# Kernel tuning notes

Hardware: AMD Instinct MI355X
Metric: run time of the kernel (lower is better)

Reference implementation:

```python
import jax, jax.numpy as jnp
import numpy as np

B, T, D, H = 8, 1024, 1024, 16
HD = D // H  # head_dim = 64


def setup_inputs() -> dict:
    key = jax.random.key(0)
    ks = jax.random.split(key, 3)
    scale = 0.02
    return {
        "x": jax.random.normal(ks[0], (B, T, D), dtype=jnp.float32),
        "w_qkv": jax.random.normal(ks[1], (D, 3 * D), dtype=jnp.float32) * scale,
        "b_qkv": jnp.zeros((3 * D,), dtype=jnp.float32),
        "w_proj": jax.random.normal(ks[2], (D, D), dtype=jnp.float32) * scale,
        "b_proj": jnp.zeros((D,), dtype=jnp.float32),
    }


def reference(x, w_qkv, b_qkv, w_proj, b_proj):
    b, t, c = x.shape
    qkv = x @ w_qkv + b_qkv                      # [B,T,3D]
    qkv = qkv.reshape(b, t, 3, H, HD)
    q, k, v = [jnp.transpose(qkv[:, :, i], (0, 2, 1, 3)) for i in range(3)]  # [B,H,T,HD]
    att = jnp.einsum("bhqd,bhkd->bhqk", q, k) / np.sqrt(HD)
    causal = jnp.triu(jnp.ones((t, t), dtype=bool), k=1)
    att = jnp.where(causal, -jnp.inf, att)
    att = jax.nn.softmax(att, axis=-1)
    out = jnp.einsum("bhqk,bhkd->bhqd", att, v)  # [B,H,T,HD]
    out = jnp.transpose(out, (0, 2, 1, 3)).reshape(b, t, c)
    return out @ w_proj + b_proj
```

## Files before the change

### kernel.cpp

```cpp
#include <hip/hip_runtime.h>
#include <hip/hip_bf16.h>

#define BATCH 8
#define SEQ   1024
#define DIM   1024
#define NH    16
#define HDIM  64
#define LDQKV 3072

typedef __attribute__((ext_vector_type(8))) short bf16x8;
typedef __attribute__((ext_vector_type(4))) float f32x4;

typedef const __attribute__((address_space(1))) void* gvptr;
typedef __attribute__((address_space(3))) void* lvptr;

static __device__ __forceinline__ short f2bf(float f) {
    unsigned u = __float_as_uint(f);
    unsigned r = (u + 0x7fffu + ((u >> 16) & 1u)) >> 16;
    return (short)r;
}
static __device__ __forceinline__ unsigned pack2bf(float lo, float hi) {
    unsigned a = __float_as_uint(lo), b = __float_as_uint(hi);
    return ((a + 0x8000u) >> 16) | ((b + 0x8000u) & 0xffff0000u);
}

__global__ __launch_bounds__(256) void cast_f2b_kernel(
    const float* __restrict__ in, short* __restrict__ out)
{
    size_t i = ((size_t)blockIdx.x * 256 + threadIdx.x) * 8;
    float4 a = *(const float4*)&in[i];
    float4 b = *(const float4*)&in[i + 4];
    bf16x8 o;
    o[0] = f2bf(a.x); o[1] = f2bf(a.y); o[2] = f2bf(a.z); o[3] = f2bf(a.w);
    o[4] = f2bf(b.x); o[5] = f2bf(b.y); o[6] = f2bf(b.z); o[7] = f2bf(b.w);
    *(bf16x8*)&out[i] = o;
}

__global__ __launch_bounds__(256) void tcast_kernel(
    const float* __restrict__ in, short* __restrict__ out, int R, int C)
{
    __shared__ float Ld[32][33];
    const int tx = threadIdx.x & 31;
    const int ty = threadIdx.x >> 5;
    const int c0 = blockIdx.x * 32;
    const int r0 = blockIdx.y * 32;
#pragma unroll
    for (int i = 0; i < 4; i++) {
        int r = ty + i * 8;
        Ld[r][tx] = in[(size_t)(r0 + r) * C + c0 + tx];
    }
    __syncthreads();
#pragma unroll
    for (int i = 0; i < 4; i++) {
        int rr = ty + i * 8;
        out[(size_t)(c0 + rr) * R + r0 + tx] = f2bf(Ld[tx][rr]);
    }
}

template<bool OUT_BF16>
__global__ __launch_bounds__(256) void gemm_mfma_kernel(
    const short* __restrict__ A,
    const short* __restrict__ Bt,
    const float* __restrict__ bias,
    void* __restrict__ Cout,
    int M, int N, int K)
{
    __shared__ __align__(16) short As[128 * 32];
    __shared__ __align__(16) short Bs[128 * 32];

    const int tid  = threadIdx.x;
    const int w    = tid >> 6;
    const int lane = tid & 63;
    const int l16  = lane & 15;
    const int quad = lane >> 4;
    const int wm   = w >> 1;
    const int wn   = w & 1;
    const int m0   = blockIdx.y * 128;
    const int n0   = blockIdx.x * 128;

    f32x4 acc[4][4];
#pragma unroll
    for (int mi = 0; mi < 4; mi++)
#pragma unroll
        for (int ni = 0; ni < 4; ni++) acc[mi][ni] = (f32x4){0.f, 0.f, 0.f, 0.f};

    for (int kt = 0; kt < K; kt += 32) {
        __syncthreads();
#pragma unroll
        for (int r = 0; r < 2; r++) {
            int vi  = tid + r * 256;
            int row = vi >> 2;
            int kb  = (vi & 3) * 8;
            __builtin_amdgcn_global_load_lds(
                (gvptr)&A[(size_t)(m0 + row) * K + kt + kb],
                (lvptr)&As[vi * 8], 16, 0, 0);
        }
#pragma unroll
        for (int r = 0; r < 2; r++) {
            int vi  = tid + r * 256;
            int row = vi >> 2;
            int kb  = (vi & 3) * 8;
            __builtin_amdgcn_global_load_lds(
                (gvptr)&Bt[(size_t)(n0 + row) * K + kt + kb],
                (lvptr)&Bs[vi * 8], 16, 0, 0);
        }
        __syncthreads();

        bf16x8 af[4], bfr[4];
#pragma unroll
        for (int mi = 0; mi < 4; mi++)
            af[mi] = *(const bf16x8*)&As[(wm * 64 + mi * 16 + l16) * 32 + quad * 8];
#pragma unroll
        for (int ni = 0; ni < 4; ni++)
            bfr[ni] = *(const bf16x8*)&Bs[(wn * 64 + ni * 16 + l16) * 32 + quad * 8];
#pragma unroll
        for (int mi = 0; mi < 4; mi++)
#pragma unroll
            for (int ni = 0; ni < 4; ni++)
                acc[mi][ni] = __builtin_amdgcn_mfma_f32_16x16x32_bf16(
                    af[mi], bfr[ni], acc[mi][ni], 0, 0, 0);
    }

#pragma unroll
    for (int ni = 0; ni < 4; ni++) {
        int n = n0 + wn * 64 + ni * 16 + l16;
        float bv = bias[n];
#pragma unroll
        for (int mi = 0; mi < 4; mi++) {
#pragma unroll
            for (int reg = 0; reg < 4; reg++) {
                int m = m0 + wm * 64 + mi * 16 + quad * 4 + reg;
                float v = acc[mi][ni][reg] + bv;
                if (OUT_BF16)
                    ((short*)Cout)[(size_t)m * N + n] = f2bf(v);
                else
                    ((float*)Cout)[(size_t)m * N + n] = v;
            }
        }
    }
}

#define LDK 72
#define LDP 72

__global__ __launch_bounds__(256, 4) void attn_kernel(
    const short* __restrict__ qkv, short* __restrict__ out)
{
    const int bh    = blockIdx.x;
    const int qtile = 7 - (int)blockIdx.y;
    const int b  = bh >> 4;
    const int h  = bh & 15;
    const int q0 = qtile * 128;
    const int tid  = threadIdx.x;
    const int w    = tid >> 6;
    const int lane = tid & 63;
    const int l16  = lane & 15;
    const int quad = lane >> 4;

    __shared__ __align__(16) short Ks[64 * LDK];
    __shared__ __align__(16) short Vt[64 * LDK];
    __shared__ __align__(16) short QP[128 * LDP];

    const short* qbase = qkv + (size_t)(b * SEQ + q0) * LDQKV + h * HDIM;
#pragma unroll
    for (int s = 0; s < 4; s++) {
        int vi = tid + s * 256;
        int row = vi >> 3, d8 = (vi & 7) * 8;
        *(bf16x8*)&QP[row * LDP + d8] =
            *(const bf16x8*)&qbase[(size_t)row * LDQKV + d8];
    }
    __syncthreads();

    bf16x8 qfragT[2][2];
#pragma unroll
    for (int qb = 0; qb < 2; qb++)
#pragma unroll
        for (int ks = 0; ks < 2; ks++)
            qfragT[qb][ks] = *(const bf16x8*)
                &QP[(w * 32 + qb * 16 + l16) * LDP + ks * 32 + quad * 8];

    f32x4 o_accT[2][4];
#pragma unroll
    for (int qb = 0; qb < 2; qb++)
#pragma unroll
        for (int db = 0; db < 4; db++) o_accT[qb][db] = (f32x4){0.f, 0.f, 0.f, 0.f};
    float l_run[2] = {0.f, 0.f};

    const int nkt = 2 * qtile + 2;
    const short* kb0 = qkv + (size_t)b * SEQ * LDQKV + DIM + h * HDIM;
    const short* vb0 = kb0 + DIM;

    const int vkey0 = (tid & 15) * 4;
    const int vd4   = (tid >> 4) * 4;

    bf16x8 kreg[2];
    short4 vreg[4];
#pragma unroll
    for (int s = 0; s < 2; s++) {
        int vi = tid + s * 256;
        kreg[s] = *(const bf16x8*)&kb0[(size_t)(vi >> 3) * LDQKV + (vi & 7) * 8];
    }
#pragma unroll
    for (int i = 0; i < 4; i++)
        vreg[i] = *(const short4*)&vb0[(size_t)(vkey0 + i) * LDQKV + vd4];
#pragma unroll
    for (int s = 0; s < 2; s++) {
        int vi = tid + s * 256;
        *(bf16x8*)&Ks[(vi >> 3) * LDK + (vi & 7) * 8] = kreg[s];
    }
    *(short4*)&Vt[(vd4 + 0) * LDK + vkey0] = make_short4(vreg[0].x, vreg[1].x, vreg[2].x, vreg[3].x);
    *(short4*)&Vt[(vd4 + 1) * LDK + vkey0] = make_short4(vreg[0].y, vreg[1].y, vreg[2].y, vreg[3].y);
    *(short4*)&Vt[(vd4 + 2) * LDK + vkey0] = make_short4(vreg[0].z, vreg[1].z, vreg[2].z, vreg[3].z);
    *(short4*)&Vt[(vd4 + 3) * LDK + vkey0] = make_short4(vreg[0].w, vreg[1].w, vreg[2].w, vreg[3].w);

    for (int kt = 0; kt < nkt; kt++) {
        __syncthreads();
        const int k0 = kt * 64;

        if (kt + 1 < nkt) {
            const short* kb = kb0 + (size_t)(k0 + 64) * LDQKV;
            const short* vb = vb0 + (size_t)(k0 + 64) * LDQKV;
#pragma unroll
            for (int s = 0; s < 2; s++) {
                int vi = tid + s * 256;
                kreg[s] = *(const bf16x8*)&kb[(size_t)(vi >> 3) * LDQKV + (vi & 7) * 8];
            }
#pragma unroll
            for (int i = 0; i < 4; i++)
                vreg[i] = *(const short4*)&vb[(size_t)(vkey0 + i) * LDQKV + vd4];
        }

        f32x4 sT[2][4];
#pragma unroll
        for (int qb = 0; qb < 2; qb++)
#pragma unroll
            for (int kb = 0; kb < 4; kb++) sT[qb][kb] = (f32x4){0.f, 0.f, 0.f, 0.f};
#pragma unroll
        for (int kb = 0; kb < 4; kb++) {
            bf16x8 kf0 = *(const bf16x8*)&Ks[(kb * 16 + l16) * LDK + quad * 8];
            bf16x8 kf1 = *(const bf16x8*)&Ks[(kb * 16 + l16) * LDK + 32 + quad * 8];
#pragma unroll
            for (int qb = 0; qb < 2; qb++) {
                sT[qb][kb] = __builtin_amdgcn_mfma_f32_16x16x32_bf16(
                    kf0, qfragT[qb][0], sT[qb][kb], 0, 0, 0);
                sT[qb][kb] = __builtin_amdgcn_mfma_f32_16x16x32_bf16(
                    kf1, qfragT[qb][1], sT[qb][kb], 0, 0, 0);
            }
        }

        const bool domask = (kt >= nkt - 2);
#pragma unroll
        for (int qb = 0; qb < 2; qb++) {
            const int q = q0 + w * 32 + qb * 16 + l16;
            float lsum = 0.f;
#pragma unroll
            for (int kb = 0; kb < 4; kb++) {
                float p[4];
#pragma unroll
                for (int r = 0; r < 4; r++) {
                    float e = __expf(sT[qb][kb][r] * 0.125f);
                    int key = k0 + kb * 16 + quad * 4 + r;
                    p[r] = (!domask || key <= q) ? e : 0.f;
                    lsum += p[r];
                }
                unsigned d0 = pack2bf(p[0], p[1]);
                unsigned d1 = pack2bf(p[2], p[3]);
                *(uint2*)&QP[(w * 32 + qb * 16 + l16) * LDP + kb * 16 + quad * 4] =
                    make_uint2(d0, d1);
            }
            lsum += __shfl_xor(lsum, 16, 64);
            lsum += __shfl_xor(lsum, 32, 64);
            l_run[qb] += lsum;
        }

#pragma unroll
        for (int ks2 = 0; ks2 < 2; ks2++) {
            bf16x8 pf[2];
#pragma unroll
            for (int qb = 0; qb < 2; qb++)
                pf[qb] = *(const bf16x8*)
                    &QP[(w * 32 + qb * 16 + l16) * LDP + ks2 * 32 + quad * 8];
#pragma unroll
            for (int db = 0; db < 4; db++) {
                bf16x8 vf = *(const bf16x8*)&Vt[(db * 16 + l16) * LDK + ks2 * 32 + quad * 8];
#pragma unroll
                for (int qb = 0; qb < 2; qb++)
                    o_accT[qb][db] = __builtin_amdgcn_mfma_f32_16x16x32_bf16(
                        vf, pf[qb], o_accT[qb][db], 0, 0, 0);
            }
        }

        __syncthreads();
        if (kt + 1 < nkt) {
#pragma unroll
            for (int s = 0; s < 2; s++) {
                int vi = tid + s * 256;
                *(bf16x8*)&Ks[(vi >> 3) * LDK + (vi & 7) * 8] = kreg[s];
            }
            *(short4*)&Vt[(vd4 + 0) * LDK + vkey0] = make_short4(vreg[0].x, vreg[1].x, vreg[2].x, vreg[3].x);
            *(short4*)&Vt[(vd4 + 1) * LDK + vkey0] = make_short4(vreg[0].y, vreg[1].y, vreg[2].y, vreg[3].y);
            *(short4*)&Vt[(vd4 + 2) * LDK + vkey0] = make_short4(vreg[0].z, vreg[1].z, vreg[2].z, vreg[3].z);
            *(short4*)&Vt[(vd4 + 3) * LDK + vkey0] = make_short4(vreg[0].w, vreg[1].w, vreg[2].w, vreg[3].w);
        }
    }

#pragma unroll
    for (int qb = 0; qb < 2; qb++) {
        const float inv = 1.f / l_run[qb];
        const int q = q0 + w * 32 + qb * 16 + l16;
        short* ob = out + (size_t)(b * SEQ + q) * DIM + h * HDIM;
#pragma unroll
        for (int db = 0; db < 4; db++) {
            float v0 = o_accT[qb][db][0] * inv;
            float v1 = o_accT[qb][db][1] * inv;
            float v2 = o_accT[qb][db][2] * inv;
            float v3 = o_accT[qb][db][3] * inv;
            *(uint2*)&ob[db * 16 + quad * 4] =
                make_uint2(pack2bf(v0, v1), pack2bf(v2, v3));
        }
    }
}

extern "C" void kernel_launch(void* const* d_in, const int* in_sizes, int n_in,
                              void* d_out, int out_size, void* d_ws, size_t ws_size,
                              hipStream_t stream)
{
    const float* x      = (const float*)d_in[0];
    const float* w_qkv  = (const float*)d_in[1];
    const float* b_qkv  = (const float*)d_in[2];
    const float* w_proj = (const float*)d_in[3];
    const float* b_proj = (const float*)d_in[4];
    float* out = (float*)d_out;

    const int M = BATCH * SEQ;

    short* xb    = (short*)d_ws;
    short* wqb   = xb   + (size_t)M * DIM;
    short* wpb   = wqb  + (size_t)LDQKV * DIM;
    short* qkvb  = wpb  + (size_t)DIM * DIM;
    short* attnb = qkvb + (size_t)M * LDQKV;

    cast_f2b_kernel<<<(M * DIM) / (256 * 8), 256, 0, stream>>>(x, xb);
    tcast_kernel<<<dim3(LDQKV / 32, DIM / 32), 256, 0, stream>>>(w_qkv, wqb, DIM, LDQKV);
    tcast_kernel<<<dim3(DIM / 32, DIM / 32), 256, 0, stream>>>(w_proj, wpb, DIM, DIM);

    gemm_mfma_kernel<true><<<dim3(LDQKV / 128, M / 128), 256, 0, stream>>>(
        xb, wqb, b_qkv, (void*)qkvb, M, LDQKV, DIM);

    attn_kernel<<<dim3(BATCH * NH, SEQ / 128), 256, 0, stream>>>(qkvb, attnb);

    gemm_mfma_kernel<false><<<dim3(DIM / 128, M / 128), 256, 0, stream>>>(
        attnb, wpb, b_proj, (void*)out, M, DIM, DIM);
}
```

Measured before the change: 237.0 us.

## Emit head-major Q/K and transposed V from QKV GEMM; double-buffer swizzled attention tiles

The QKV GEMM epilogue now scatters its output into per-head contiguous Q and K buffers and a pre-transposed V buffer. The attention kernel can then load K/V tiles with contiguous 16-byte loads instead of doing a strided register transpose. The attention kernel keeps double-buffered, XOR-swizzled LDS tiles for K and V, which removes one barrier per iteration and the padding, and uses exp2 with a folded scale. The three prep/cast kernels are merged into one launch. In exchange, the GEMM epilogue does scattered 2-byte stores for Q/K, and the higher LDS use lowers the occupancy hint from 4 to 3.

Result: no change. 239.2 us (+0.9%).

```diff
diff --git a/kernel.cpp b/kernel.cpp
--- a/kernel.cpp
+++ b/kernel.cpp
@@ -24,26 +24,31 @@
     return ((a + 0x8000u) >> 16) | ((b + 0x8000u) & 0xffff0000u);
 }
 
-__global__ __launch_bounds__(256) void cast_f2b_kernel(
-    const float* __restrict__ in, short* __restrict__ out)
+__global__ __launch_bounds__(256) void prep_kernel(
+    const float* __restrict__ x, const float* __restrict__ wq,
+    const float* __restrict__ wp,
+    short* __restrict__ xb, short* __restrict__ wqb, short* __restrict__ wpb)
 {
-    size_t i = ((size_t)blockIdx.x * 256 + threadIdx.x) * 8;
-    float4 a = *(const float4*)&in[i];
-    float4 b = *(const float4*)&in[i + 4];
-    bf16x8 o;
-    o[0] = f2bf(a.x); o[1] = f2bf(a.y); o[2] = f2bf(a.z); o[3] = f2bf(a.w);
-    o[4] = f2bf(b.x); o[5] = f2bf(b.y); o[6] = f2bf(b.z); o[7] = f2bf(b.w);
-    *(bf16x8*)&out[i] = o;
-}
-
-__global__ __launch_bounds__(256) void tcast_kernel(
-    const float* __restrict__ in, short* __restrict__ out, int R, int C)
-{
+    const int bid = blockIdx.x;
+    const int tid = threadIdx.x;
+    if (bid < 4096) {
+        size_t i = ((size_t)bid * 256 + tid) * 8;
+        float4 a = *(const float4*)&x[i];
+        float4 b = *(const float4*)&x[i + 4];
+        bf16x8 o;
+        o[0] = f2bf(a.x); o[1] = f2bf(a.y); o[2] = f2bf(a.z); o[3] = f2bf(a.w);
+        o[4] = f2bf(b.x); o[5] = f2bf(b.y); o[6] = f2bf(b.z); o[7] = f2bf(b.w);
+        *(bf16x8*)&xb[i] = o;
+        return;
+    }
     __shared__ float Ld[32][33];
-    const int tx = threadIdx.x & 31;
-    const int ty = threadIdx.x >> 5;
-    const int c0 = blockIdx.x * 32;
-    const int r0 = blockIdx.y * 32;
+    const float* in; short* outp; int C, tb;
+    if (bid < 4096 + 3072) { tb = bid - 4096; in = wq; outp = wqb; C = LDQKV; }
+    else                   { tb = bid - 7168; in = wp; outp = wpb; C = DIM; }
+    const int R = DIM;
+    const int ntx = C / 32;
+    const int c0 = (tb % ntx) * 32, r0 = (tb / ntx) * 32;
+    const int tx = tid & 31, ty = tid >> 5;
 #pragma unroll
     for (int i = 0; i < 4; i++) {
         int r = ty + i * 8;
@@ -53,16 +58,17 @@
 #pragma unroll
     for (int i = 0; i < 4; i++) {
         int rr = ty + i * 8;
-        out[(size_t)(c0 + rr) * R + r0 + tx] = f2bf(Ld[tx][rr]);
-    }
-}
-
-template<bool OUT_BF16>
+        outp[(size_t)(c0 + rr) * R + r0 + tx] = f2bf(Ld[tx][rr]);
+    }
+}
+
+template<int MODE>
 __global__ __launch_bounds__(256) void gemm_mfma_kernel(
     const short* __restrict__ A,
     const short* __restrict__ Bt,
     const float* __restrict__ bias,
-    void* __restrict__ Cout,
+    float* __restrict__ Cf,
+    short* __restrict__ Qh, short* __restrict__ Kh, short* __restrict__ Vth,
     int M, int N, int K)
 {
     __shared__ __align__(16) short As[128 * 32];
@@ -121,30 +127,61 @@
                     af[mi], bfr[ni], acc[mi][ni], 0, 0, 0);
     }
 
-#pragma unroll
-    for (int ni = 0; ni < 4; ni++) {
-        int n = n0 + wn * 64 + ni * 16 + l16;
-        float bv = bias[n];
-#pragma unroll
-        for (int mi = 0; mi < 4; mi++) {
-#pragma unroll
-            for (int reg = 0; reg < 4; reg++) {
-                int m = m0 + wm * 64 + mi * 16 + quad * 4 + reg;
-                float v = acc[mi][ni][reg] + bv;
-                if (OUT_BF16)
-                    ((short*)Cout)[(size_t)m * N + n] = f2bf(v);
-                else
-                    ((float*)Cout)[(size_t)m * N + n] = v;
+    if (MODE == 0) {
+#pragma unroll
+        for (int ni = 0; ni < 4; ni++) {
+            int n = n0 + wn * 64 + ni * 16 + l16;
+            float bv = bias[n];
+#pragma unroll
+            for (int mi = 0; mi < 4; mi++)
+#pragma unroll
+                for (int reg = 0; reg < 4; reg++) {
+                    int m = m0 + wm * 64 + mi * 16 + quad * 4 + reg;
+                    Cf[(size_t)m * N + n] = acc[mi][ni][reg] + bv;
+                }
+        }
+    } else {
+        const int b16 = (m0 >> 10) * 16;
+        const int tB  = m0 & 1023;
+        const int sec = n0 >> 10;
+#pragma unroll
+        for (int ni = 0; ni < 4; ni++) {
+            int n  = n0 + wn * 64 + ni * 16 + l16;
+            int nl = n & 1023;
+            int hh = nl >> 6, dd = nl & 63;
+            float bv = bias[n];
+            size_t base = (size_t)(b16 + hh) * (SEQ * HDIM);
+            if (sec == 2) {
+#pragma unroll
+                for (int mi = 0; mi < 4; mi++) {
+                    int t0 = tB + wm * 64 + mi * 16 + quad * 4;
+                    float v0 = acc[mi][ni][0] + bv;
+                    float v1 = acc[mi][ni][1] + bv;
+                    float v2 = acc[mi][ni][2] + bv;
+                    float v3 = acc[mi][ni][3] + bv;
+                    *(uint2*)&Vth[base + (size_t)dd * SEQ + t0] =
+                        make_uint2(pack2bf(v0, v1), pack2bf(v2, v3));
+                }
+            } else {
+                short* dst = (sec == 0) ? Qh : Kh;
+#pragma unroll
+                for (int mi = 0; mi < 4; mi++)
+#pragma unroll
+                    for (int reg = 0; reg < 4; reg++) {
+                        int t = tB + wm * 64 + mi * 16 + quad * 4 + reg;
+                        dst[base + (size_t)t * HDIM + dd] =
+                            f2bf(acc[mi][ni][reg] + bv);
+                    }
             }
         }
     }
 }
 
-#define LDK 72
 #define LDP 72
 
-__global__ __launch_bounds__(256, 4) void attn_kernel(
-    const short* __restrict__ qkv, short* __restrict__ out)
+__global__ __launch_bounds__(256, 3) void attn_kernel(
+    const short* __restrict__ Qh, const short* __restrict__ Kh,
+    const short* __restrict__ Vth, short* __restrict__ out)
 {
     const int bh    = blockIdx.x;
     const int qtile = 7 - (int)blockIdx.y;
@@ -156,18 +193,18 @@
     const int lane = tid & 63;
     const int l16  = lane & 15;
     const int quad = lane >> 4;
-
-    __shared__ __align__(16) short Ks[64 * LDK];
-    __shared__ __align__(16) short Vt[64 * LDK];
+    const int sw   = l16 & 7;
+
+    __shared__ __align__(16) short KsB[2 * 64 * 64];
+    __shared__ __align__(16) short VtB[2 * 64 * 64];
     __shared__ __align__(16) short QP[128 * LDP];
 
-    const short* qbase = qkv + (size_t)(b * SEQ + q0) * LDQKV + h * HDIM;
+    const short* qbase = Qh + (size_t)bh * (SEQ * HDIM) + (size_t)q0 * HDIM;
 #pragma unroll
     for (int s = 0; s < 4; s++) {
         int vi = tid + s * 256;
         int row = vi >> 3, d8 = (vi & 7) * 8;
-        *(bf16x8*)&QP[row * LDP + d8] =
-            *(const bf16x8*)&qbase[(size_t)row * LDQKV + d8];
+        *(bf16x8*)&QP[row * LDP + d8] = *(const bf16x8*)&qbase[row * HDIM + d8];
     }
     __syncthreads();
 
@@ -187,47 +224,37 @@
     float l_run[2] = {0.f, 0.f};
 
     const int nkt = 2 * qtile + 2;
-    const short* kb0 = qkv + (size_t)b * SEQ * LDQKV + DIM + h * HDIM;
-    const short* vb0 = kb0 + DIM;
-
-    const int vkey0 = (tid & 15) * 4;
-    const int vd4   = (tid >> 4) * 4;
-
-    bf16x8 kreg[2];
-    short4 vreg[4];
-#pragma unroll
-    for (int s = 0; s < 2; s++) {
-        int vi = tid + s * 256;
-        kreg[s] = *(const bf16x8*)&kb0[(size_t)(vi >> 3) * LDQKV + (vi & 7) * 8];
-    }
-#pragma unroll
-    for (int i = 0; i < 4; i++)
-        vreg[i] = *(const short4*)&vb0[(size_t)(vkey0 + i) * LDQKV + vd4];
-#pragma unroll
-    for (int s = 0; s < 2; s++) {
-        int vi = tid + s * 256;
-        *(bf16x8*)&Ks[(vi >> 3) * LDK + (vi & 7) * 8] = kreg[s];
-    }
-    *(short4*)&Vt[(vd4 + 0) * LDK + vkey0] = make_short4(vreg[0].x, vreg[1].x, vreg[2].x, vreg[3].x);
-    *(short4*)&Vt[(vd4 + 1) * LDK + vkey0] = make_short4(vreg[0].y, vreg[1].y, vreg[2].y, vreg[3].y);
-    *(short4*)&Vt[(vd4 + 2) * LDK + vkey0] = make_short4(vreg[0].z, vreg[1].z, vreg[2].z, vreg[3].z);
-    *(short4*)&Vt[(vd4 + 3) * LDK + vkey0] = make_short4(vreg[0].w, vreg[1].w, vreg[2].w, vreg[3].w);
+    const short* kb0 = Kh  + (size_t)bh * (SEQ * HDIM);
+    const short* vb0 = Vth + (size_t)bh * (SEQ * HDIM);
+
+    const int srow = tid >> 3;
+    const int sch  = tid & 7;
+    const int sslot0 = (sch ^ (srow & 7)) * 8;
+    const int sslot1 = (sch ^ ((srow + 32) & 7)) * 8;
+
+    bf16x8 kreg[2], vreg[2];
+    kreg[0] = *(const bf16x8*)&kb0[(size_t)srow * HDIM + sch * 8];
+    kreg[1] = *(const bf16x8*)&kb0[(size_t)(srow + 32) * HDIM + sch * 8];
+    vreg[0] = *(const bf16x8*)&vb0[(size_t)srow * SEQ + sch * 8];
+    vreg[1] = *(const bf16x8*)&vb0[(size_t)(srow + 32) * SEQ + sch * 8];
+    *(bf16x8*)&KsB[srow * 64 + sslot0]        = kreg[0];
+    *(bf16x8*)&KsB[(srow + 32) * 64 + sslot1] = kreg[1];
+    *(bf16x8*)&VtB[srow * 64 + sslot0]        = vreg[0];
+    *(bf16x8*)&VtB[(srow + 32) * 64 + sslot1] = vreg[1];
 
     for (int kt = 0; kt < nkt; kt++) {
         __syncthreads();
         const int k0 = kt * 64;
+        const short* Ks = &KsB[(kt & 1) * 4096];
+        const short* Vt = &VtB[(kt & 1) * 4096];
 
         if (kt + 1 < nkt) {
-            const short* kb = kb0 + (size_t)(k0 + 64) * LDQKV;
-            const short* vb = vb0 + (size_t)(k0 + 64) * LDQKV;
-#pragma unroll
-            for (int s = 0; s < 2; s++) {
-                int vi = tid + s * 256;
-                kreg[s] = *(const bf16x8*)&kb[(size_t)(vi >> 3) * LDQKV + (vi & 7) * 8];
-            }
-#pragma unroll
-            for (int i = 0; i < 4; i++)
-                vreg[i] = *(const short4*)&vb[(size_t)(vkey0 + i) * LDQKV + vd4];
+            const short* kb = kb0 + (size_t)(k0 + 64) * HDIM;
+            const short* vb = vb0 + (k0 + 64);
+            kreg[0] = *(const bf16x8*)&kb[(size_t)srow * HDIM + sch * 8];
+            kreg[1] = *(const bf16x8*)&kb[(size_t)(srow + 32) * HDIM + sch * 8];
+            vreg[0] = *(const bf16x8*)&vb[(size_t)srow * SEQ + sch * 8];
+            vreg[1] = *(const bf16x8*)&vb[(size_t)(srow + 32) * SEQ + sch * 8];
         }
 
         f32x4 sT[2][4];
@@ -237,8 +264,8 @@
             for (int kb = 0; kb < 4; kb++) sT[qb][kb] = (f32x4){0.f, 0.f, 0.f, 0.f};
 #pragma unroll
         for (int kb = 0; kb < 4; kb++) {
-            bf16x8 kf0 = *(const bf16x8*)&Ks[(kb * 16 + l16) * LDK + quad * 8];
-            bf16x8 kf1 = *(const bf16x8*)&Ks[(kb * 16 + l16) * LDK + 32 + quad * 8];
+            bf16x8 kf0 = *(const bf16x8*)&Ks[(kb * 16 + l16) * 64 + ((0 + quad) ^ sw) * 8];
+            bf16x8 kf1 = *(const bf16x8*)&Ks[(kb * 16 + l16) * 64 + ((4 + quad) ^ sw) * 8];
 #pragma unroll
             for (int qb = 0; qb < 2; qb++) {
                 sT[qb][kb] = __builtin_amdgcn_mfma_f32_16x16x32_bf16(
@@ -249,6 +276,7 @@
         }
 
         const bool domask = (kt >= nkt - 2);
+        const float c2 = 0.18033688011112042f;
 #pragma unroll
         for (int qb = 0; qb < 2; qb++) {
             const int q = q0 + w * 32 + qb * 16 + l16;
@@ -258,15 +286,13 @@
                 float p[4];
 #pragma unroll
                 for (int r = 0; r < 4; r++) {
-                    float e = __expf(sT[qb][kb][r] * 0.125f);
+                    float e = exp2f(sT[qb][kb][r] * c2);
                     int key = k0 + kb * 16 + quad * 4 + r;
                     p[r] = (!domask || key <= q) ? e : 0.f;
                     lsum += p[r];
                 }
-                unsigned d0 = pack2bf(p[0], p[1]);
-                unsigned d1 = pack2bf(p[2], p[3]);
                 *(uint2*)&QP[(w * 32 + qb * 16 + l16) * LDP + kb * 16 + quad * 4] =
-                    make_uint2(d0, d1);
+                    make_uint2(pack2bf(p[0], p[1]), pack2bf(p[2], p[3]));
             }
             lsum += __shfl_xor(lsum, 16, 64);
             lsum += __shfl_xor(lsum, 32, 64);
@@ -282,7 +308,8 @@
                     &QP[(w * 32 + qb * 16 + l16) * LDP + ks2 * 32 + quad * 8];
 #pragma unroll
             for (int db = 0; db < 4; db++) {
-                bf16x8 vf = *(const bf16x8*)&Vt[(db * 16 + l16) * LDK + ks2 * 32 + quad * 8];
+                bf16x8 vf = *(const bf16x8*)
+                    &Vt[(db * 16 + l16) * 64 + ((ks2 * 4 + quad) ^ sw) * 8];
 #pragma unroll
                 for (int qb = 0; qb < 2; qb++)
                     o_accT[qb][db] = __builtin_amdgcn_mfma_f32_16x16x32_bf16(
@@ -290,17 +317,13 @@
             }
         }
 
-        __syncthreads();
         if (kt + 1 < nkt) {
-#pragma unroll
-            for (int s = 0; s < 2; s++) {
-                int vi = tid + s * 256;
-                *(bf16x8*)&Ks[(vi >> 3) * LDK + (vi & 7) * 8] = kreg[s];
-            }
-            *(short4*)&Vt[(vd4 + 0) * LDK + vkey0] = make_short4(vreg[0].x, vreg[1].x, vreg[2].x, vreg[3].x);
-            *(short4*)&Vt[(vd4 + 1) * LDK + vkey0] = make_short4(vreg[0].y, vreg[1].y, vreg[2].y, vreg[3].y);
-            *(short4*)&Vt[(vd4 + 2) * LDK + vkey0] = make_short4(vreg[0].z, vreg[1].z, vreg[2].z, vreg[3].z);
-            *(short4*)&Vt[(vd4 + 3) * LDK + vkey0] = make_short4(vreg[0].w, vreg[1].w, vreg[2].w, vreg[3].w);
+            short* Kn = &KsB[((kt + 1) & 1) * 4096];
+            short* Vn = &VtB[((kt + 1) & 1) * 4096];
+            *(bf16x8*)&Kn[srow * 64 + sslot0]        = kreg[0];
+            *(bf16x8*)&Kn[(srow + 32) * 64 + sslot1] = kreg[1];
+            *(bf16x8*)&Vn[srow * 64 + sslot0]        = vreg[0];
+            *(bf16x8*)&Vn[(srow + 32) * 64 + sslot1] = vreg[1];
         }
     }
 
@@ -335,20 +358,21 @@
     const int M = BATCH * SEQ;
 
     short* xb    = (short*)d_ws;
-    short* wqb   = xb   + (size_t)M * DIM;
-    short* wpb   = wqb  + (size_t)LDQKV * DIM;
-    short* qkvb  = wpb  + (size_t)DIM * DIM;
-    short* attnb = qkvb + (size_t)M * LDQKV;
-
-    cast_f2b_kernel<<<(M * DIM) / (256 * 8), 256, 0, stream>>>(x, xb);
-    tcast_kernel<<<dim3(LDQKV / 32, DIM / 32), 256, 0, stream>>>(w_qkv, wqb, DIM, LDQKV);
-    tcast_kernel<<<dim3(DIM / 32, DIM / 32), 256, 0, stream>>>(w_proj, wpb, DIM, DIM);
-
-    gemm_mfma_kernel<true><<<dim3(LDQKV / 128, M / 128), 256, 0, stream>>>(
-        xb, wqb, b_qkv, (void*)qkvb, M, LDQKV, DIM);
-
-    attn_kernel<<<dim3(BATCH * NH, SEQ / 128), 256, 0, stream>>>(qkvb, attnb);
-
-    gemm_mfma_kernel<false><<<dim3(DIM / 128, M / 128), 256, 0, stream>>>(
-        attnb, wpb, b_proj, (void*)out, M, DIM, DIM);
-}
+    short* wqb   = xb    + (size_t)M * DIM;
+    short* wpb   = wqb   + (size_t)LDQKV * DIM;
+    short* Qhb   = wpb   + (size_t)DIM * DIM;
+    short* Khb   = Qhb   + (size_t)M * DIM;
+    short* Vthb  = Khb   + (size_t)M * DIM;
+    short* attnb = Vthb  + (size_t)M * DIM;
+
+    prep_kernel<<<8192, 256, 0, stream>>>(x, w_qkv, w_proj, xb, wqb, wpb);
+
+    gemm_mfma_kernel<1><<<dim3(LDQKV / 128, M / 128), 256, 0, stream>>>(
+        xb, wqb, b_qkv, nullptr, Qhb, Khb, Vthb, M, LDQKV, DIM);
+
+    attn_kernel<<<dim3(BATCH * NH, SEQ / 128), 256, 0, stream>>>(
+        Qhb, Khb, Vthb, attnb);
+
+    gemm_mfma_kernel<0><<<dim3(DIM / 128, M / 128), 256, 0, stream>>>(
+        attnb, wpb, b_proj, out, nullptr, nullptr, nullptr, M, DIM, DIM);
+}
```
